# Kernel tuning notes

Measured on AMD Instinct MI355X. Metric: run time of the kernel, lower is better.

Reference implementation:

```python
import jax, jax.numpy as jnp
import numpy as np

B, D, H = 16384, 1024, 16
HD = D // H
EPS = 1e-5


def setup_inputs() -> dict:
    key = jax.random.key(0)
    ks = jax.random.split(key, 16)
    w = lambda k, shape: jax.random.normal(k, shape, jnp.float32) * 0.02
    return {
        "img_emb": jax.random.normal(ks[0], (B, D), jnp.float32),
        "txt_emb": jax.random.normal(ks[1], (B, D), jnp.float32),
        "route_choice": jax.random.randint(ks[2], (B,), 0, 3, jnp.int32),
        # gate: Linear(2D -> D) + sigmoid
        "Wg": w(ks[3], (2 * D, D)), "bg": jnp.zeros((D,), jnp.float32),
        # MultiheadAttention in/out projections
        "Wqkv": w(ks[4], (D, 3 * D)), "bqkv": jnp.zeros((3 * D,), jnp.float32),
        "Wo": w(ks[5], (D, D)), "bo": jnp.zeros((D,), jnp.float32),
        # LayerNorm
        "gamma": jnp.ones((D,), jnp.float32), "beta": jnp.zeros((D,), jnp.float32),
        # FFN: Linear(D->4D), GELU, Linear(4D->D)
        "Wf1": w(ks[6], (D, 4 * D)), "bf1": jnp.zeros((4 * D,), jnp.float32),
        "Wf2": w(ks[7], (4 * D, D)), "bf2": jnp.zeros((D,), jnp.float32),
    }


def _layernorm(x, gamma, beta):
    mu = jnp.mean(x, axis=-1, keepdims=True)
    var = jnp.mean(jnp.square(x - mu), axis=-1, keepdims=True)
    return (x - mu) * jax.lax.rsqrt(var + EPS) * gamma + beta


def reference(img_emb, txt_emb, route_choice, Wg, bg, Wqkv, bqkv, Wo, bo,
              gamma, beta, Wf1, bf1, Wf2, bf2):
    # Eval mode: energy_loss = 0, no dropout. Routing choice supplied as int input.
    # Compute the 'full' fusion branch densely, then select per sample.
    ri = jnp.concatenate([img_emb, txt_emb], axis=-1)          # [B, 2D]
    gate = jax.nn.sigmoid(ri @ Wg + bg)                        # [B, D]
    fused = gate * img_emb + (1.0 - gate) * txt_emb            # [B, D]

    x = jnp.stack([img_emb, txt_emb], axis=1)                  # [B, 2, D]
    qkv = x @ Wqkv + bqkv                                      # [B, 2, 3D]
    q, k, v = jnp.split(qkv, 3, axis=-1)
    q = q.reshape(B, 2, H, HD)
    k = k.reshape(B, 2, H, HD)
    v = v.reshape(B, 2, H, HD)
    scores = jnp.einsum("bqhd,bkhd->bhqk", q, k) / np.sqrt(HD) # [B, H, 2, 2]
    attn = jax.nn.softmax(scores, axis=-1)
    ctx = jnp.einsum("bhqk,bkhd->bqhd", attn, v).reshape(B, 2, D)
    attn_out = ctx @ Wo + bo                                   # [B, 2, D]

    fused = fused + attn_out.mean(axis=1)
    fused = _layernorm(fused, gamma, beta)
    full_out = jax.nn.gelu(fused @ Wf1 + bf1, approximate=False) @ Wf2 + bf2

    rc = route_choice[:, None]
    out = jnp.where(rc == 0, img_emb, jnp.where(rc == 1, txt_emb, full_out))
    return out
```

## Files before the change

kernel.cpp:

```cpp
#include <hip/hip_runtime.h>
#include <hip/hip_bf16.h>
#include <math.h>

#define NB 16384
#define DIM 1024
#define CAP 6656
#define MT 52

using bf16 = __hip_bfloat16;
typedef __attribute__((ext_vector_type(8))) short short8;
typedef __attribute__((ext_vector_type(4))) short short4v;
typedef __attribute__((ext_vector_type(4))) float float4v;

__device__ __forceinline__ void gl_lds16(const void* g, void* l) {
  __builtin_amdgcn_global_load_lds(
      (const __attribute__((address_space(1))) unsigned int*)g,
      (__attribute__((address_space(3))) unsigned int*)l, 16, 0, 0);
}

__device__ __forceinline__ short f2bf(float x) {
  __hip_bfloat16 h = __float2bfloat16(x);
  return *reinterpret_cast<short*>(&h);
}

__device__ __forceinline__ void swz(int bid, int nN, int& m0, int& n0) {
  int x = bid & 7;
  int r = bid >> 3;
  int nl = nN >> 3;
  int nLoc = r % nl;
  int m = r / nl;
  n0 = (x + 8 * nLoc) * 128;
  m0 = m * 128;
}

__global__ __launch_bounds__(256) void transpose_cast(
    const float* __restrict__ in, bf16* __restrict__ out, int K, int N) {
  __shared__ float tile[32][33];
  int n0 = blockIdx.x * 32, k0 = blockIdx.y * 32;
  int tx = threadIdx.x, ty = threadIdx.y;
#pragma unroll
  for (int i = 0; i < 32; i += 8)
    tile[ty + i][tx] = in[(size_t)(k0 + ty + i) * N + n0 + tx];
  __syncthreads();
#pragma unroll
  for (int i = 0; i < 32; i += 8)
    out[(size_t)(n0 + ty + i) * K + k0 + tx] = __float2bfloat16(tile[tx][ty + i]);
}

__global__ __launch_bounds__(256) void fill_bias(const float* __restrict__ bqkv,
                                                 const float* __restrict__ bg,
                                                 float* __restrict__ biasA,
                                                 float* __restrict__ biasB) {
  int i = blockIdx.x * 256 + threadIdx.x;
  float qv = (i < 3072) ? bqkv[i] : 0.f;
  biasA[i] = qv;
  biasB[i] = (i < 3072) ? qv : bg[i - 3072];
}

__global__ void zero_cnt(int* cnt) { if (threadIdx.x == 0) *cnt = 0; }

__global__ __launch_bounds__(256) void index_build(const int* __restrict__ route,
                                                   int* __restrict__ cnt,
                                                   int* __restrict__ idx,
                                                   int* __restrict__ pos) {
  int r = blockIdx.x * 256 + threadIdx.x;
  if (r < NB && route[r] == 2) {
    int p = atomicAdd(cnt, 1);
    idx[p] = r;
    pos[r] = p;
  }
}

__global__ __launch_bounds__(256) void gather_cast(
    const float* __restrict__ img, const float* __restrict__ txt,
    const int* __restrict__ cnt, const int* __restrict__ idx,
    bf16* __restrict__ xg, bf16* __restrict__ tg) {
  int n = blockIdx.x;
  if (n >= *cnt) return;
  int r = idx[n];
  int c = threadIdx.x * 4;
  float4 vi = *(const float4*)(img + (size_t)r * DIM + c);
  float4 vt = *(const float4*)(txt + (size_t)r * DIM + c);
  short4v pi, pt;
  pi[0] = f2bf(vi.x); pi[1] = f2bf(vi.y); pi[2] = f2bf(vi.z); pi[3] = f2bf(vi.w);
  pt[0] = f2bf(vt.x); pt[1] = f2bf(vt.y); pt[2] = f2bf(vt.z); pt[3] = f2bf(vt.w);
  *(short4v*)(xg + (size_t)n * DIM + c) = pi;
  *(short4v*)(tg + (size_t)n * DIM + c) = pt;
}

__global__ __launch_bounds__(256) void gemm_qkvg(
    const bf16* __restrict__ A0, const bf16* __restrict__ BtQ,
    const bf16* __restrict__ BtG, const float* __restrict__ bias,
    bf16* __restrict__ outp, const int* __restrict__ cntp) {
  const int cnt = *cntp;
  int m0, n0;
  swz(blockIdx.x, 32, m0, n0);
  if (m0 >= ((cnt + 127) & ~127)) return;
  alignas(16) __shared__ bf16 sA[128 * 32];
  alignas(16) __shared__ bf16 sB[128 * 32];
  const int t = threadIdx.x;
  const int wave = t >> 6, lane = t & 63;
  const int wm = (wave >> 1) * 64, wn = (wave & 1) * 64;
  const int r16 = lane & 15, quad = lane >> 4;
  const bf16* Bt = (n0 < 3072) ? BtQ + (size_t)n0 * 1024 : BtG + (size_t)(n0 - 3072) * 1024;

  float4v acc[4][4] = {};
  for (int k0 = 0; k0 < 1024; k0 += 32) {
    if (k0) __syncthreads();
#pragma unroll
    for (int j = 0; j < 2; ++j) {
      int c = t + j * 256;
      int row = c >> 2;
      int kk = k0 + (c & 3) * 8;
      gl_lds16(Bt + (size_t)row * 1024 + kk, (void*)(sB + j * 2048 + wave * 512));
      gl_lds16(A0 + (size_t)(m0 + row) * 1024 + kk, (void*)(sA + j * 2048 + wave * 512));
    }
    __syncthreads();
    short8 af[4], bfr[4];
#pragma unroll
    for (int i = 0; i < 4; ++i) {
      af[i] = *(const short8*)(sA + (wm + i * 16 + r16) * 32 + quad * 8);
      bfr[i] = *(const short8*)(sB + (wn + i * 16 + r16) * 32 + quad * 8);
    }
#pragma unroll
    for (int i = 0; i < 4; ++i)
#pragma unroll
      for (int j = 0; j < 4; ++j)
        acc[i][j] =
            __builtin_amdgcn_mfma_f32_16x16x32_bf16(af[i], bfr[j], acc[i][j], 0, 0, 0);
  }
#pragma unroll
  for (int i = 0; i < 4; ++i)
#pragma unroll
    for (int j = 0; j < 4; ++j) {
      int gcol = n0 + wn + j * 16 + r16;
      float bv = bias[gcol];
#pragma unroll
      for (int r = 0; r < 4; ++r) {
        int grow = m0 + wm + i * 16 + quad * 4 + r;
        outp[(size_t)grow * 4096 + gcol] = __float2bfloat16(acc[i][j][r] + bv);
      }
    }
}

__global__ __launch_bounds__(256) void attn_kernel(const bf16* __restrict__ qx,
                                                   const bf16* __restrict__ tx,
                                                   bf16* __restrict__ cmean,
                                                   const int* __restrict__ cntp) {
  const int cnt = *cntp;
  int gw = blockIdx.x * 4 + (threadIdx.x >> 6);
  int lane = threadIdx.x & 63;
  int n = gw >> 4, h = gw & 15;
  if (n >= ((cnt + 127) & ~127)) return;
  const bf16* b0 = qx + (size_t)n * 4096 + h * 64 + lane;
  const bf16* b1 = tx + (size_t)n * 4096 + h * 64 + lane;
  float q0 = __bfloat162float(b0[0]);
  float k0 = __bfloat162float(b0[1024]);
  float v0 = __bfloat162float(b0[2048]);
  float q1 = __bfloat162float(b1[0]);
  float k1 = __bfloat162float(b1[1024]);
  float v1 = __bfloat162float(b1[2048]);
  float s00 = q0 * k0, s01 = q0 * k1, s10 = q1 * k0, s11 = q1 * k1;
#pragma unroll
  for (int d = 32; d > 0; d >>= 1) {
    s00 += __shfl_xor(s00, d);
    s01 += __shfl_xor(s01, d);
    s10 += __shfl_xor(s10, d);
    s11 += __shfl_xor(s11, d);
  }
  const float sc = 0.125f;
  s00 *= sc; s01 *= sc; s10 *= sc; s11 *= sc;
  float m0 = fmaxf(s00, s01), m1 = fmaxf(s10, s11);
  float e00 = expf(s00 - m0), e01 = expf(s01 - m0);
  float e10 = expf(s10 - m1), e11 = expf(s11 - m1);
  float i0 = 1.f / (e00 + e01), i1 = 1.f / (e10 + e11);
  float c0 = (e00 * i0) * v0 + (e01 * i0) * v1;
  float c1 = (e10 * i1) * v0 + (e11 * i1) * v1;
  cmean[(size_t)n * DIM + h * 64 + lane] = __float2bfloat16(0.5f * (c0 + c1));
}

__global__ __launch_bounds__(256) void wo_z_kernel(
    const float* __restrict__ img, const float* __restrict__ txt,
    const bf16* __restrict__ qx, const bf16* __restrict__ tx,
    const bf16* __restrict__ WoT, const float* __restrict__ bg,
    const float* __restrict__ bo, const bf16* __restrict__ cmean,
    bf16* __restrict__ z, const int* __restrict__ cntp, const int* __restrict__ idx) {
  const int cnt = *cntp;
  int m0, n0;
  swz(blockIdx.x, 8, m0, n0);
  if (m0 >= ((cnt + 127) & ~127)) return;
  alignas(16) __shared__ bf16 sA[128 * 32];
  alignas(16) __shared__ bf16 sB[128 * 32];
  const int t = threadIdx.x;
  const int wave = t >> 6, lane = t & 63;
  const int wm = (wave >> 1) * 64, wn = (wave & 1) * 64;
  const int r16 = lane & 15, quad = lane >> 4;

  float4v acc[4][4] = {};
  for (int k0 = 0; k0 < 1024; k0 += 32) {
    if (k0) __syncthreads();
#pragma unroll
    for (int j = 0; j < 2; ++j) {
      int c = t + j * 256;
      int row = c >> 2;
      int kk = k0 + (c & 3) * 8;
      gl_lds16(WoT + (size_t)(n0 + row) * 1024 + kk, (void*)(sB + j * 2048 + wave * 512));
      gl_lds16(cmean + (size_t)(m0 + row) * 1024 + kk, (void*)(sA + j * 2048 + wave * 512));
    }
    __syncthreads();
    short8 af[4], bfr[4];
#pragma unroll
    for (int i = 0; i < 4; ++i) {
      af[i] = *(const short8*)(sA + (wm + i * 16 + r16) * 32 + quad * 8);
      bfr[i] = *(const short8*)(sB + (wn + i * 16 + r16) * 32 + quad * 8);
    }
#pragma unroll
    for (int i = 0; i < 4; ++i)
#pragma unroll
      for (int j = 0; j < 4; ++j)
        acc[i][j] =
            __builtin_amdgcn_mfma_f32_16x16x32_bf16(af[i], bfr[j], acc[i][j], 0, 0, 0);
  }
#pragma unroll
  for (int i = 0; i < 4; ++i)
#pragma unroll
    for (int j = 0; j < 4; ++j) {
      int gcol = n0 + wn + j * 16 + r16;
      float bgv = bg[gcol], bov = bo[gcol];
#pragma unroll
      for (int r = 0; r < 4; ++r) {
        int grow = m0 + wm + i * 16 + quad * 4 + r;
        float zv = 0.f;
        if (grow < cnt) {
          int orow = idx[grow];
          float gp = __bfloat162float(qx[(size_t)grow * 4096 + 3072 + gcol]) +
                     __bfloat162float(tx[(size_t)grow * 4096 + 3072 + gcol]) + bgv;
          float g = 1.f / (1.f + expf(-gp));
          size_t ii = (size_t)orow * DIM + gcol;
          float fm = g * img[ii] + (1.f - g) * txt[ii];
          zv = fm + acc[i][j][r] + bov;
        }
        z[(size_t)grow * DIM + gcol] = __float2bfloat16(zv);
      }
    }
}

__global__ __launch_bounds__(256) void ln_kernel(bf16* __restrict__ z,
                                                 const float* __restrict__ g,
                                                 const float* __restrict__ be,
                                                 const int* __restrict__ cntp) {
  const int cnt = *cntp;
  int b = blockIdx.x, t = threadIdx.x;
  if (b >= ((cnt + 127) & ~127)) return;
  bf16* zr = z + (size_t)b * DIM;
  float v[4];
  float s = 0.f, s2 = 0.f;
#pragma unroll
  for (int i = 0; i < 4; ++i) {
    float x = __bfloat162float(zr[t + 256 * i]);
    v[i] = x; s += x; s2 += x * x;
  }
#pragma unroll
  for (int d = 32; d > 0; d >>= 1) {
    s += __shfl_xor(s, d);
    s2 += __shfl_xor(s2, d);
  }
  __shared__ float rs[4], rs2[4];
  int w = t >> 6, lane = t & 63;
  if (!lane) { rs[w] = s; rs2[w] = s2; }
  __syncthreads();
  s = rs[0] + rs[1] + rs[2] + rs[3];
  s2 = rs2[0] + rs2[1] + rs2[2] + rs2[3];
  float mu = s * (1.f / 1024.f);
  float var = s2 * (1.f / 1024.f) - mu * mu;
  float r = rsqrtf(var + 1e-5f);
#pragma unroll
  for (int i = 0; i < 4; ++i) {
    int c = t + 256 * i;
    zr[c] = __float2bfloat16((v[i] - mu) * r * g[c] + be[c]);
  }
}

__global__ __launch_bounds__(256) void gemm_gelu(
    const bf16* __restrict__ A0, const bf16* __restrict__ Bt,
    const float* __restrict__ bias, bf16* __restrict__ outp,
    const int* __restrict__ cntp) {
  const int cnt = *cntp;
  int m0, n0;
  swz(blockIdx.x, 32, m0, n0);
  if (m0 >= ((cnt + 127) & ~127)) return;
  alignas(16) __shared__ bf16 sA[128 * 32];
  alignas(16) __shared__ bf16 sB[128 * 32];
  const int t = threadIdx.x;
  const int wave = t >> 6, lane = t & 63;
  const int wm = (wave >> 1) * 64, wn = (wave & 1) * 64;
  const int r16 = lane & 15, quad = lane >> 4;

  float4v acc[4][4] = {};
  for (int k0 = 0; k0 < 1024; k0 += 32) {
    if (k0) __syncthreads();
#pragma unroll
    for (int j = 0; j < 2; ++j) {
      int c = t + j * 256;
      int row = c >> 2;
      int kk = k0 + (c & 3) * 8;
      gl_lds16(Bt + (size_t)(n0 + row) * 1024 + kk, (void*)(sB + j * 2048 + wave * 512));
      gl_lds16(A0 + (size_t)(m0 + row) * 1024 + kk, (void*)(sA + j * 2048 + wave * 512));
    }
    __syncthreads();
    short8 af[4], bfr[4];
#pragma unroll
    for (int i = 0; i < 4; ++i) {
      af[i] = *(const short8*)(sA + (wm + i * 16 + r16) * 32 + quad * 8);
      bfr[i] = *(const short8*)(sB + (wn + i * 16 + r16) * 32 + quad * 8);
    }
#pragma unroll
    for (int i = 0; i < 4; ++i)
#pragma unroll
      for (int j = 0; j < 4; ++j)
        acc[i][j] =
            __builtin_amdgcn_mfma_f32_16x16x32_bf16(af[i], bfr[j], acc[i][j], 0, 0, 0);
  }
#pragma unroll
  for (int i = 0; i < 4; ++i)
#pragma unroll
    for (int j = 0; j < 4; ++j) {
      int gcol = n0 + wn + j * 16 + r16;
      float bv = bias[gcol];
#pragma unroll
      for (int r = 0; r < 4; ++r) {
        int grow = m0 + wm + i * 16 + quad * 4 + r;
        float v = acc[i][j][r] + bv;
        float gl = 0.5f * v * (1.f + erff(v * 0.70710678118654752f));
        outp[(size_t)grow * 4096 + gcol] = __float2bfloat16(gl);
      }
    }
}

__global__ __launch_bounds__(256) void gemm_splitk(
    const bf16* __restrict__ A0, const bf16* __restrict__ Bt,
    float* __restrict__ parts, const int* __restrict__ cntp) {
  const int cnt = *cntp;
  const int nblk = 8 * MT;
  int s = blockIdx.x / nblk;
  int bid = blockIdx.x % nblk;
  int m0, n0;
  swz(bid, 8, m0, n0);
  if (m0 >= ((cnt + 127) & ~127)) return;
  alignas(16) __shared__ bf16 sA[128 * 32];
  alignas(16) __shared__ bf16 sB[128 * 32];
  const int t = threadIdx.x;
  const int wave = t >> 6, lane = t & 63;
  const int wm = (wave >> 1) * 64, wn = (wave & 1) * 64;
  const int r16 = lane & 15, quad = lane >> 4;
  const int kbase = s * 2048;

  float4v acc[4][4] = {};
  for (int k0 = kbase; k0 < kbase + 2048; k0 += 32) {
    if (k0 != kbase) __syncthreads();
#pragma unroll
    for (int j = 0; j < 2; ++j) {
      int c = t + j * 256;
      int row = c >> 2;
      int kk = k0 + (c & 3) * 8;
      gl_lds16(Bt + (size_t)(n0 + row) * 4096 + kk, (void*)(sB + j * 2048 + wave * 512));
      gl_lds16(A0 + (size_t)(m0 + row) * 4096 + kk, (void*)(sA + j * 2048 + wave * 512));
    }
    __syncthreads();
    short8 af[4], bfr[4];
#pragma unroll
    for (int i = 0; i < 4; ++i) {
      af[i] = *(const short8*)(sA + (wm + i * 16 + r16) * 32 + quad * 8);
      bfr[i] = *(const short8*)(sB + (wn + i * 16 + r16) * 32 + quad * 8);
    }
#pragma unroll
    for (int i = 0; i < 4; ++i)
#pragma unroll
      for (int j = 0; j < 4; ++j)
        acc[i][j] =
            __builtin_amdgcn_mfma_f32_16x16x32_bf16(af[i], bfr[j], acc[i][j], 0, 0, 0);
  }
  float* out = parts + (size_t)s * CAP * 1024;
#pragma unroll
  for (int i = 0; i < 4; ++i)
#pragma unroll
    for (int j = 0; j < 4; ++j) {
      int gcol = n0 + wn + j * 16 + r16;
#pragma unroll
      for (int r = 0; r < 4; ++r) {
        int grow = m0 + wm + i * 16 + quad * 4 + r;
        out[(size_t)grow * 1024 + gcol] = acc[i][j][r];
      }
    }
}

__global__ __launch_bounds__(256) void route_out(
    const float* __restrict__ img, const float* __restrict__ txt,
    const int* __restrict__ route, const int* __restrict__ pos,
    const float* __restrict__ parts, const float* __restrict__ bf2,
    float* __restrict__ out) {
  int row = blockIdx.x;
  int rc = route[row];
  int c = threadIdx.x * 4;
  float4 v;
  if (rc == 2) {
    int n = pos[row];
    float4 p0 = *(const float4*)(parts + (size_t)n * 1024 + c);
    float4 p1 = *(const float4*)(parts + (size_t)CAP * 1024 + (size_t)n * 1024 + c);
    float4 b = *(const float4*)(bf2 + c);
    v.x = p0.x + p1.x + b.x;
    v.y = p0.y + p1.y + b.y;
    v.z = p0.z + p1.z + b.z;
    v.w = p0.w + p1.w + b.w;
  } else {
    const float* src = (rc == 0) ? img : txt;
    v = *(const float4*)(src + (size_t)row * DIM + c);
  }
  *(float4*)(out + (size_t)row * DIM + c) = v;
}

extern "C" void kernel_launch(void* const* d_in, const int* in_sizes, int n_in,
                              void* d_out, int out_size, void* d_ws, size_t ws_size,
                              hipStream_t stream) {
  const float* img = (const float*)d_in[0];
  const float* txt = (const float*)d_in[1];
  const int* route = (const int*)d_in[2];
  const float* Wg = (const float*)d_in[3];
  const float* bg = (const float*)d_in[4];
  const float* Wqkv = (const float*)d_in[5];
  const float* bqkv = (const float*)d_in[6];
  const float* Wo = (const float*)d_in[7];
  const float* bo = (const float*)d_in[8];
  const float* gamma = (const float*)d_in[9];
  const float* beta = (const float*)d_in[10];
  const float* Wf1 = (const float*)d_in[11];
  const float* bf1 = (const float*)d_in[12];
  const float* Wf2 = (const float*)d_in[13];
  const float* bf2 = (const float*)d_in[14];

  char* ws = (char*)d_ws;
  size_t off = 0;
  auto alloc = [&](size_t bytes) {
    char* p = ws + off;
    off += (bytes + 255) & ~(size_t)255;
    return p;
  };
  int* cntp = (int*)alloc(256);
  int* idx = (int*)alloc((size_t)NB * 4);
  int* pos = (int*)alloc((size_t)NB * 4);
  float* biasA = (float*)alloc(4096 * 4);
  float* biasB = (float*)alloc(4096 * 4);
  bf16* WqkvT = (bf16*)alloc((size_t)3072 * 1024 * 2);
  bf16* WgTopT = (bf16*)alloc((size_t)1024 * 1024 * 2);
  bf16* WgBotT = (bf16*)alloc((size_t)1024 * 1024 * 2);
  bf16* WoT = (bf16*)alloc((size_t)1024 * 1024 * 2);
  bf16* Wf1T = (bf16*)alloc((size_t)4096 * 1024 * 2);
  bf16* Wf2T = (bf16*)alloc((size_t)1024 * 4096 * 2);
  bf16* xg = (bf16*)alloc((size_t)CAP * 1024 * 2);
  bf16* tg = (bf16*)alloc((size_t)CAP * 1024 * 2);
  bf16* qx = (bf16*)alloc((size_t)CAP * 4096 * 2);
  bf16* tx = (bf16*)alloc((size_t)CAP * 4096 * 2);
  bf16* cmean = (bf16*)alloc((size_t)CAP * 1024 * 2);
  bf16* zb = (bf16*)alloc((size_t)CAP * 1024 * 2);
  bf16* hb = qx;
  float* parts = (float*)tx;

  dim3 tblk(32, 8);
  transpose_cast<<<dim3(3072 / 32, 1024 / 32), tblk, 0, stream>>>(Wqkv, WqkvT, 1024, 3072);
  transpose_cast<<<dim3(1024 / 32, 1024 / 32), tblk, 0, stream>>>(Wg, WgTopT, 1024, 1024);
  transpose_cast<<<dim3(1024 / 32, 1024 / 32), tblk, 0, stream>>>(Wg + 1024 * 1024, WgBotT, 1024, 1024);
  transpose_cast<<<dim3(1024 / 32, 1024 / 32), tblk, 0, stream>>>(Wo, WoT, 1024, 1024);
  transpose_cast<<<dim3(4096 / 32, 1024 / 32), tblk, 0, stream>>>(Wf1, Wf1T, 1024, 4096);
  transpose_cast<<<dim3(1024 / 32, 4096 / 32), tblk, 0, stream>>>(Wf2, Wf2T, 4096, 1024);
  fill_bias<<<16, 256, 0, stream>>>(bqkv, bg, biasA, biasB);

  zero_cnt<<<1, 64, 0, stream>>>(cntp);
  index_build<<<NB / 256, 256, 0, stream>>>(route, cntp, idx, pos);
  gather_cast<<<CAP, 256, 0, stream>>>(img, txt, cntp, idx, xg, tg);

  gemm_qkvg<<<32 * MT, 256, 0, stream>>>(xg, WqkvT, WgTopT, biasA, qx, cntp);
  gemm_qkvg<<<32 * MT, 256, 0, stream>>>(tg, WqkvT, WgBotT, biasB, tx, cntp);
  attn_kernel<<<CAP * 4, 256, 0, stream>>>(qx, tx, cmean, cntp);
  wo_z_kernel<<<8 * MT, 256, 0, stream>>>(img, txt, qx, tx, WoT, bg, bo, cmean, zb,
                                          cntp, idx);
  ln_kernel<<<CAP, 256, 0, stream>>>(zb, gamma, beta, cntp);
  gemm_gelu<<<32 * MT, 256, 0, stream>>>(zb, Wf1T, bf1, hb, cntp);
  gemm_splitk<<<2 * 8 * MT, 256, 0, stream>>>(hb, Wf2T, parts, cntp);
  route_out<<<NB, 256, 0, stream>>>(img, txt, route, pos, parts, bf2, (float*)d_out);
}
```

Before: 597.0 us.

## Replace 128x128 GEMMs with pipelined 256x256 tiled GEMM template

Three separate 128x128 single-buffered GEMM kernels give way to one templated 256x256-tile kernel with 512 threads. It uses a 4-slot LDS ring with 3-deep prefetch, XOR-swizzled LDS layout, setprio around MFMAs and explicit waitcnt/barrier scheduling. The two QKV+gate GEMMs are merged into one launch. The goal is more data reuse per tile and overlap of global loads with MFMA work, at the cost of larger LDS/register use and coarser padding of rows to 256.

```diff
diff --git a/kernel.cpp b/kernel.cpp
--- a/kernel.cpp
+++ b/kernel.cpp
@@ -6,6 +6,7 @@
 #define DIM 1024
 #define CAP 6656
 #define MT 52
+#define MT2 26
 
 using bf16 = __hip_bfloat16;
 typedef __attribute__((ext_vector_type(8))) short short8;
@@ -31,6 +32,161 @@
   int m = r / nl;
   n0 = (x + 8 * nLoc) * 128;
   m0 = m * 128;
+}
+
+__device__ __forceinline__ void swz256(int bid, int nN, int& m0, int& n0) {
+  int x = bid & 7;
+  int r = bid >> 3;
+  int nl = nN >> 3;
+  n0 = (x + 8 * (r % nl)) * 256;
+  m0 = (r / nl) * 256;
+}
+
+__device__ __forceinline__ void stage_unit(const bf16* __restrict__ gbase,
+                                           int ld, int kc, bf16* ubase, int t) {
+#pragma unroll
+  for (int j = 0; j < 2; ++j) {
+    int ch = t + j * 512;
+    int rg = ch >> 6;
+    int q = (ch & 63) * 16;
+    q ^= ((q >> 9) & 1) << 5;
+    const bf16* src =
+        gbase + (size_t)(rg * 16 + (q >> 6)) * ld + kc + ((q & 63) >> 1);
+    gl_lds16(src, (void*)(ubase + ((t >> 6) << 9) + j * 4096));
+  }
+}
+
+template <int MODE>
+__global__ __launch_bounds__(512, 2) void gemm256(
+    const bf16* __restrict__ A0, const bf16* __restrict__ A1,
+    const bf16* __restrict__ B0, const bf16* __restrict__ Bg0,
+    const bf16* __restrict__ Bg1, const float* __restrict__ bias0,
+    const float* __restrict__ bias1, bf16* __restrict__ O0,
+    bf16* __restrict__ O1, float* __restrict__ P,
+    const int* __restrict__ cntp) {
+  const int cnt = *cntp;
+  int bid = blockIdx.x;
+  int g = 0, sk = 0, m0, n0;
+  if constexpr (MODE == 0) {
+    g = bid >= 416;
+    bid -= g * 416;
+    swz256(bid, 16, m0, n0);
+  } else if constexpr (MODE == 1) {
+    swz256(bid, 16, m0, n0);
+  } else {
+    sk = bid / 104;
+    int rm = bid % 104;
+    m0 = (rm >> 2) * 256;
+    n0 = (rm & 3) * 256;
+  }
+  if (m0 >= ((cnt + 255) & ~255)) return;
+
+  constexpr int LDA = (MODE == 2) ? 4096 : 1024;
+  constexpr int LDB = (MODE == 2) ? 4096 : 1024;
+  constexpr int NIT = (MODE == 2) ? 16 : 8;
+  const int kb = (MODE == 2) ? sk * 2048 : 0;
+
+  const bf16* Ab;
+  const bf16* Bt;
+  if constexpr (MODE == 0) {
+    Ab = (g ? A1 : A0) + (size_t)m0 * LDA;
+    Bt = (n0 < 3072) ? B0 + (size_t)n0 * 1024
+                     : (g ? Bg1 : Bg0) + (size_t)(n0 - 3072) * 1024;
+  } else {
+    Ab = A0 + (size_t)m0 * LDA;
+    Bt = B0 + (size_t)n0 * LDB;
+  }
+
+  alignas(16) __shared__ bf16 lds[4][2][8192];
+  const int t = threadIdx.x;
+  const int wave = t >> 6, lane = t & 63;
+  const int wm = wave >> 2, wn = wave & 3;
+  const int r16 = lane & 15, quad = lane >> 4;
+  const int aoff = ((r16 * 64 + quad * 16) ^ ((r16 & 8) << 2)) >> 1;
+
+#pragma unroll
+  for (int s = 0; s < 3; ++s) {
+    stage_unit(Ab, LDA, kb + s * 32, &lds[s][0][0], t);
+    stage_unit(Bt, LDB, kb + s * 32, &lds[s][1][0], t);
+  }
+  asm volatile("s_waitcnt vmcnt(8)" ::: "memory");
+  __builtin_amdgcn_s_barrier();
+
+  float4v acc[8][4] = {};
+  for (int it = 0; it < NIT; ++it) {
+#pragma unroll
+    for (int ph = 0; ph < 8; ++ph) {
+      const int tau = it * 4 + (ph >> 1);
+      const int slot = tau & 3;
+      const int mq = ph & 1;
+      short8 av[4], bv[4];
+      const bf16* aU = &lds[slot][0][0];
+      const bf16* bU = &lds[slot][1][0];
+#pragma unroll
+      for (int mi = 0; mi < 4; ++mi)
+        av[mi] = *(const short8*)(aU + (wm * 8 + mq * 4 + mi) * 512 + aoff);
+#pragma unroll
+      for (int ni = 0; ni < 4; ++ni)
+        bv[ni] = *(const short8*)(bU + (wn * 4 + ni) * 512 + aoff);
+      if ((ph & 1) == 0) {
+        const int sg = tau + 3;
+        if (sg < NIT * 4) {
+          const int sl = sg & 3;
+          stage_unit(Ab, LDA, kb + sg * 32, &lds[sl][0][0], t);
+          stage_unit(Bt, LDB, kb + sg * 32, &lds[sl][1][0], t);
+        }
+      }
+      __builtin_amdgcn_s_barrier();
+      asm volatile("s_waitcnt lgkmcnt(0)" ::: "memory");
+      __builtin_amdgcn_s_setprio(1);
+#pragma unroll
+      for (int mi = 0; mi < 4; ++mi)
+#pragma unroll
+        for (int ni = 0; ni < 4; ++ni)
+          acc[mq * 4 + mi][ni] = __builtin_amdgcn_mfma_f32_16x16x32_bf16(
+              av[mi], bv[ni], acc[mq * 4 + mi][ni], 0, 0, 0);
+      __builtin_amdgcn_s_setprio(0);
+      if (ph == 3 || ph == 7)
+        asm volatile("s_waitcnt vmcnt(4)" ::: "memory");
+      __builtin_amdgcn_s_barrier();
+    }
+  }
+
+  const int colb = n0 + wn * 64 + r16;
+  if constexpr (MODE == 2) {
+    float* out = P + (size_t)sk * CAP * 1024;
+#pragma unroll
+    for (int nf = 0; nf < 4; ++nf) {
+      int gcol = colb + nf * 16;
+#pragma unroll
+      for (int mf = 0; mf < 8; ++mf)
+#pragma unroll
+        for (int r = 0; r < 4; ++r) {
+          int grow = m0 + wm * 128 + mf * 16 + quad * 4 + r;
+          out[(size_t)grow * 1024 + gcol] = acc[mf][nf][r];
+        }
+    }
+  } else {
+    const float* bias = (MODE == 0) ? (g ? bias1 : bias0) : bias0;
+    bf16* O = (MODE == 0) ? (g ? O1 : O0) : O0;
+    float bvv[4];
+#pragma unroll
+    for (int nf = 0; nf < 4; ++nf) bvv[nf] = bias[colb + nf * 16];
+#pragma unroll
+    for (int nf = 0; nf < 4; ++nf) {
+      int gcol = colb + nf * 16;
+#pragma unroll
+      for (int mf = 0; mf < 8; ++mf)
+#pragma unroll
+        for (int r = 0; r < 4; ++r) {
+          int grow = m0 + wm * 128 + mf * 16 + quad * 4 + r;
+          float v = acc[mf][nf][r] + bvv[nf];
+          if constexpr (MODE == 1)
+            v = 0.5f * v * (1.f + erff(v * 0.70710678118654752f));
+          O[(size_t)grow * 4096 + gcol] = __float2bfloat16(v);
+        }
+    }
+  }
 }
 
 __global__ __launch_bounds__(256) void transpose_cast(
@@ -86,61 +242,6 @@
   pt[0] = f2bf(vt.x); pt[1] = f2bf(vt.y); pt[2] = f2bf(vt.z); pt[3] = f2bf(vt.w);
   *(short4v*)(xg + (size_t)n * DIM + c) = pi;
   *(short4v*)(tg + (size_t)n * DIM + c) = pt;
-}
-
-__global__ __launch_bounds__(256) void gemm_qkvg(
-    const bf16* __restrict__ A0, const bf16* __restrict__ BtQ,
-    const bf16* __restrict__ BtG, const float* __restrict__ bias,
-    bf16* __restrict__ outp, const int* __restrict__ cntp) {
-  const int cnt = *cntp;
-  int m0, n0;
-  swz(blockIdx.x, 32, m0, n0);
-  if (m0 >= ((cnt + 127) & ~127)) return;
-  alignas(16) __shared__ bf16 sA[128 * 32];
-  alignas(16) __shared__ bf16 sB[128 * 32];
-  const int t = threadIdx.x;
-  const int wave = t >> 6, lane = t & 63;
-  const int wm = (wave >> 1) * 64, wn = (wave & 1) * 64;
-  const int r16 = lane & 15, quad = lane >> 4;
-  const bf16* Bt = (n0 < 3072) ? BtQ + (size_t)n0 * 1024 : BtG + (size_t)(n0 - 3072) * 1024;
-
-  float4v acc[4][4] = {};
-  for (int k0 = 0; k0 < 1024; k0 += 32) {
-    if (k0) __syncthreads();
-#pragma unroll
-    for (int j = 0; j < 2; ++j) {
-      int c = t + j * 256;
-      int row = c >> 2;
-      int kk = k0 + (c & 3) * 8;
-      gl_lds16(Bt + (size_t)row * 1024 + kk, (void*)(sB + j * 2048 + wave * 512));
-      gl_lds16(A0 + (size_t)(m0 + row) * 1024 + kk, (void*)(sA + j * 2048 + wave * 512));
-    }
-    __syncthreads();
-    short8 af[4], bfr[4];
-#pragma unroll
-    for (int i = 0; i < 4; ++i) {
-      af[i] = *(const short8*)(sA + (wm + i * 16 + r16) * 32 + quad * 8);
-      bfr[i] = *(const short8*)(sB + (wn + i * 16 + r16) * 32 + quad * 8);
-    }
-#pragma unroll
-    for (int i = 0; i < 4; ++i)
-#pragma unroll
-      for (int j = 0; j < 4; ++j)
-        acc[i][j] =
-            __builtin_amdgcn_mfma_f32_16x16x32_bf16(af[i], bfr[j], acc[i][j], 0, 0, 0);
-  }
-#pragma unroll
-  for (int i = 0; i < 4; ++i)
-#pragma unroll
-    for (int j = 0; j < 4; ++j) {
-      int gcol = n0 + wn + j * 16 + r16;
-      float bv = bias[gcol];
-#pragma unroll
-      for (int r = 0; r < 4; ++r) {
-        int grow = m0 + wm + i * 16 + quad * 4 + r;
-        outp[(size_t)grow * 4096 + gcol] = __float2bfloat16(acc[i][j][r] + bv);
-      }
-    }
 }
 
 __global__ __launch_bounds__(256) void attn_kernel(const bf16* __restrict__ qx,
@@ -279,119 +380,6 @@
     int c = t + 256 * i;
     zr[c] = __float2bfloat16((v[i] - mu) * r * g[c] + be[c]);
   }
-}
-
-__global__ __launch_bounds__(256) void gemm_gelu(
-    const bf16* __restrict__ A0, const bf16* __restrict__ Bt,
-    const float* __restrict__ bias, bf16* __restrict__ outp,
-    const int* __restrict__ cntp) {
-  const int cnt = *cntp;
-  int m0, n0;
-  swz(blockIdx.x, 32, m0, n0);
-  if (m0 >= ((cnt + 127) & ~127)) return;
-  alignas(16) __shared__ bf16 sA[128 * 32];
-  alignas(16) __shared__ bf16 sB[128 * 32];
-  const int t = threadIdx.x;
-  const int wave = t >> 6, lane = t & 63;
-  const int wm = (wave >> 1) * 64, wn = (wave & 1) * 64;
-  const int r16 = lane & 15, quad = lane >> 4;
-
-  float4v acc[4][4] = {};
-  for (int k0 = 0; k0 < 1024; k0 += 32) {
-    if (k0) __syncthreads();
-#pragma unroll
-    for (int j = 0; j < 2; ++j) {
-      int c = t + j * 256;
-      int row = c >> 2;
-      int kk = k0 + (c & 3) * 8;
-      gl_lds16(Bt + (size_t)(n0 + row) * 1024 + kk, (void*)(sB + j * 2048 + wave * 512));
-      gl_lds16(A0 + (size_t)(m0 + row) * 1024 + kk, (void*)(sA + j * 2048 + wave * 512));
-    }
-    __syncthreads();
-    short8 af[4], bfr[4];
-#pragma unroll
-    for (int i = 0; i < 4; ++i) {
-      af[i] = *(const short8*)(sA + (wm + i * 16 + r16) * 32 + quad * 8);
-      bfr[i] = *(const short8*)(sB + (wn + i * 16 + r16) * 32 + quad * 8);
-    }
-#pragma unroll
-    for (int i = 0; i < 4; ++i)
-#pragma unroll
-      for (int j = 0; j < 4; ++j)
-        acc[i][j] =
-            __builtin_amdgcn_mfma_f32_16x16x32_bf16(af[i], bfr[j], acc[i][j], 0, 0, 0);
-  }
-#pragma unroll
-  for (int i = 0; i < 4; ++i)
-#pragma unroll
-    for (int j = 0; j < 4; ++j) {
-      int gcol = n0 + wn + j * 16 + r16;
-      float bv = bias[gcol];
-#pragma unroll
-      for (int r = 0; r < 4; ++r) {
-        int grow = m0 + wm + i * 16 + quad * 4 + r;
-        float v = acc[i][j][r] + bv;
-        float gl = 0.5f * v * (1.f + erff(v * 0.70710678118654752f));
-        outp[(size_t)grow * 4096 + gcol] = __float2bfloat16(gl);
-      }
-    }
-}
-
-__global__ __launch_bounds__(256) void gemm_splitk(
-    const bf16* __restrict__ A0, const bf16* __restrict__ Bt,
-    float* __restrict__ parts, const int* __restrict__ cntp) {
-  const int cnt = *cntp;
-  const int nblk = 8 * MT;
-  int s = blockIdx.x / nblk;
-  int bid = blockIdx.x % nblk;
-  int m0, n0;
-  swz(bid, 8, m0, n0);
-  if (m0 >= ((cnt + 127) & ~127)) return;
-  alignas(16) __shared__ bf16 sA[128 * 32];
-  alignas(16) __shared__ bf16 sB[128 * 32];
-  const int t = threadIdx.x;
-  const int wave = t >> 6, lane = t & 63;
-  const int wm = (wave >> 1) * 64, wn = (wave & 1) * 64;
-  const int r16 = lane & 15, quad = lane >> 4;
-  const int kbase = s * 2048;
-
-  float4v acc[4][4] = {};
-  for (int k0 = kbase; k0 < kbase + 2048; k0 += 32) {
-    if (k0 != kbase) __syncthreads();
-#pragma unroll
-    for (int j = 0; j < 2; ++j) {
-      int c = t + j * 256;
-      int row = c >> 2;
-      int kk = k0 + (c & 3) * 8;
-      gl_lds16(Bt + (size_t)(n0 + row) * 4096 + kk, (void*)(sB + j * 2048 + wave * 512));
-      gl_lds16(A0 + (size_t)(m0 + row) * 4096 + kk, (void*)(sA + j * 2048 + wave * 512));
-    }
-    __syncthreads();
-    short8 af[4], bfr[4];
-#pragma unroll
-    for (int i = 0; i < 4; ++i) {
-      af[i] = *(const short8*)(sA + (wm + i * 16 + r16) * 32 + quad * 8);
-      bfr[i] = *(const short8*)(sB + (wn + i * 16 + r16) * 32 + quad * 8);
-    }
-#pragma unroll
-    for (int i = 0; i < 4; ++i)
-#pragma unroll
-      for (int j = 0; j < 4; ++j)
-        acc[i][j] =
-            __builtin_amdgcn_mfma_f32_16x16x32_bf16(af[i], bfr[j], acc[i][j], 0, 0, 0);
-  }
-  float* out = parts + (size_t)s * CAP * 1024;
-#pragma unroll
-  for (int i = 0; i < 4; ++i)
-#pragma unroll
-    for (int j = 0; j < 4; ++j) {
-      int gcol = n0 + wn + j * 16 + r16;
-#pragma unroll
-      for (int r = 0; r < 4; ++r) {
-        int grow = m0 + wm + i * 16 + quad * 4 + r;
-        out[(size_t)grow * 1024 + gcol] = acc[i][j][r];
-      }
-    }
 }
 
 __global__ __launch_bounds__(256) void route_out(
@@ -478,13 +466,16 @@
   index_build<<<NB / 256, 256, 0, stream>>>(route, cntp, idx, pos);
   gather_cast<<<CAP, 256, 0, stream>>>(img, txt, cntp, idx, xg, tg);
 
-  gemm_qkvg<<<32 * MT, 256, 0, stream>>>(xg, WqkvT, WgTopT, biasA, qx, cntp);
-  gemm_qkvg<<<32 * MT, 256, 0, stream>>>(tg, WqkvT, WgBotT, biasB, tx, cntp);
+  gemm256<0><<<2 * MT2 * 16, 512, 0, stream>>>(xg, tg, WqkvT, WgTopT, WgBotT,
+                                               biasA, biasB, qx, tx, nullptr, cntp);
   attn_kernel<<<CAP * 4, 256, 0, stream>>>(qx, tx, cmean, cntp);
   wo_z_kernel<<<8 * MT, 256, 0, stream>>>(img, txt, qx, tx, WoT, bg, bo, cmean, zb,
                                           cntp, idx);
   ln_kernel<<<CAP, 256, 0, stream>>>(zb, gamma, beta, cntp);
-  gemm_gelu<<<32 * MT, 256, 0, stream>>>(zb, Wf1T, bf1, hb, cntp);
-  gemm_splitk<<<2 * 8 * MT, 256, 0, stream>>>(hb, Wf2T, parts, cntp);
+  gemm256<1><<<MT2 * 16, 512, 0, stream>>>(zb, nullptr, Wf1T, nullptr, nullptr,
+                                           bf1, nullptr, hb, nullptr, nullptr, cntp);
+  gemm256<2><<<MT2 * 4 * 2, 512, 0, stream>>>(hb, nullptr, Wf2T, nullptr, nullptr,
+                                              nullptr, nullptr, nullptr, nullptr,
+                                              parts, cntp);
   route_out<<<NB, 256, 0, stream>>>(img, txt, route, pos, parts, bf2, (float*)d_out);
 }
```

After: 629.1 us. 1.05x slower.
